# Optimization experiments

Hardware: AMD Instinct MI355X
Metric: run time of the kernel (lower is better)

The kernel has to match this reference:

```python
import jax, jax.numpy as jnp
import numpy as np

N_QUBITS = 10
N_LAYERS = 4
BATCH = 2048


def setup_inputs() -> dict:
    key = jax.random.key(0)
    k1, k2 = jax.random.split(key)
    x = jax.random.normal(k1, (BATCH, N_QUBITS), dtype=jnp.float32)
    q_params = jax.random.normal(k2, (N_LAYERS * N_QUBITS * 3,), dtype=jnp.float32) * 0.01
    return {"x": x, "q_params": q_params}


def _apply_1q(state, U, wire):
    # state: (B, 2, 2, ..., 2); U: (2, 2) complex. Applies U on `wire`.
    s = jnp.moveaxis(state, wire + 1, -1)
    s = jnp.einsum('...j,ij->...i', s, U)
    return jnp.moveaxis(s, -1, wire + 1)


def _apply_cnot(state, ctrl, tgt):
    # flip target amplitude pair where control bit == 1
    s = jnp.moveaxis(state, (ctrl + 1, tgt + 1), (-2, -1))
    s = jnp.concatenate([s[..., 0:1, :], s[..., 1:2, ::-1]], axis=-2)
    return jnp.moveaxis(s, (-2, -1), (ctrl + 1, tgt + 1))


def _forward(x, q_params):
    B = x.shape[0]
    n, L = N_QUBITS, N_LAYERS
    # --- data-encoding layer: RY(x_i)|0> = [cos(x_i/2), sin(x_i/2)] per qubit ---
    half = 0.5 * x
    amps = jnp.stack([jnp.cos(half), jnp.sin(half)], axis=-1).astype(jnp.complex64)  # (B, n, 2)
    state = amps[:, 0, :]
    for i in range(1, n):  # build product state via successive kron (loop over n_qubits only)
        state = (state[:, :, None] * amps[:, i, None, :]).reshape(B, -1)
    state = state.reshape((B,) + (2,) * n)
    # --- variational gate matrices: per (layer, qubit) fused U = RZ @ RY @ RX ---
    w = q_params.reshape(L, n, 3)
    c, s = jnp.cos(0.5 * w), jnp.sin(0.5 * w)
    cx = c[..., 0].astype(jnp.complex64); sx = s[..., 0].astype(jnp.complex64)
    cy = c[..., 1].astype(jnp.complex64); sy = s[..., 1].astype(jnp.complex64)
    ez = jnp.exp(-0.5j * w[..., 2].astype(jnp.complex64))
    zeros = jnp.zeros_like(ez)
    Urx = jnp.stack([jnp.stack([cx, -1j * sx], -1), jnp.stack([-1j * sx, cx], -1)], -2)  # (L,n,2,2)
    Ury = jnp.stack([jnp.stack([cy, -sy], -1), jnp.stack([sy, cy], -1)], -2)
    Urz = jnp.stack([jnp.stack([ez, zeros], -1), jnp.stack([zeros, jnp.conj(ez)], -1)], -2)
    U = jnp.einsum('lnab,lnbc,lncd->lnad', Urz, Ury, Urx)  # apply order: RX then RY then RZ
    # --- circuit layers ---
    for l in range(L):
        for i in range(n):
            state = _apply_1q(state, U[l, i], i)
        for i in range(n - 1):
            state = _apply_cnot(state, i, i + 1)
    # --- <Z_i> expectation values ---
    p = jnp.abs(state) ** 2  # (B, 2, ..., 2) real probabilities
    evs = []
    for i in range(n):
        axes = tuple(a for a in range(1, n + 1) if a != i + 1)
        pi = jnp.sum(p, axis=axes)  # (B, 2)
        evs.append(pi[:, 0] - pi[:, 1])
    return jnp.stack(evs, axis=-1)  # (B, n_qubits)


def reference(x, q_params):
    return _forward(x, q_params)
```

## Files before the change

### kernel.cpp

```cpp
#include <hip/hip_runtime.h>
#include <math.h>

#define NQ 10
#define NL 4
#define NGATES (NL * NQ)
#define NTHREADS 256
#define WPB 4

typedef float f32x2 __attribute__((ext_vector_type(2)));

#if __has_builtin(__builtin_amdgcn_permlane32_swap)
#define HAVE_PL32 1
#else
#define HAVE_PL32 0
#endif
#if __has_builtin(__builtin_amdgcn_permlane16_swap)
#define HAVE_PL16 1
#else
#define HAVE_PL16 0
#endif


template<int XM>
__device__ __forceinline__ float exch1(float v, bool sp32, bool sp16) {
    if constexpr (XM == 0) return v;
    int x = __float_as_int(v);
    constexpr int low = XM & 31;
    if constexpr (low == 1)       x = __builtin_amdgcn_mov_dpp(x, 0xB1, 0xF, 0xF, true);
    else if constexpr (low == 2)  x = __builtin_amdgcn_mov_dpp(x, 0x4E, 0xF, 0xF, true);
    else if constexpr (low == 3)  x = __builtin_amdgcn_mov_dpp(x, 0x1B, 0xF, 0xF, true);
    else if constexpr (low == 7)  x = __builtin_amdgcn_mov_dpp(x, 0x141, 0xF, 0xF, true);
    else if constexpr (low == 8)  x = __builtin_amdgcn_mov_dpp(x, 0x128, 0xF, 0xF, true);
    else if constexpr (low == 9)  { x = __builtin_amdgcn_mov_dpp(x, 0x128, 0xF, 0xF, true);
                                    x = __builtin_amdgcn_mov_dpp(x, 0xB1, 0xF, 0xF, true); }
    else if constexpr (low == 10) { x = __builtin_amdgcn_mov_dpp(x, 0x128, 0xF, 0xF, true);
                                    x = __builtin_amdgcn_mov_dpp(x, 0x4E, 0xF, 0xF, true); }
    else if constexpr (low == 11) { x = __builtin_amdgcn_mov_dpp(x, 0x128, 0xF, 0xF, true);
                                    x = __builtin_amdgcn_mov_dpp(x, 0x1B, 0xF, 0xF, true); }
    else if constexpr (low == 15) x = __builtin_amdgcn_mov_dpp(x, 0x140, 0xF, 0xF, true);
    else if constexpr (low == 16) {
#if HAVE_PL16
        auto r = __builtin_amdgcn_permlane16_swap((unsigned)x, (unsigned)x, false, false);
        x = sp16 ? (int)r[0] : (int)r[1];
#else
        x = __builtin_amdgcn_ds_swizzle(x, (16 << 10) | 0x1F);
#endif
    }
    else if constexpr (low != 0)  x = __builtin_amdgcn_ds_swizzle(x, (low << 10) | 0x1F);
    if constexpr ((XM & 32) != 0) {
#if HAVE_PL32
        auto r = __builtin_amdgcn_permlane32_swap((unsigned)x, (unsigned)x, false, false);
        x = sp32 ? (int)r[0] : (int)r[1];
#else
        x = __float_as_int(__shfl_xor(__int_as_float(x), 32, 64));
#endif
    }
    return __int_as_float(x);
}

template<int XM>
__device__ __forceinline__ f32x2 exch2(f32x2 v, bool sp32, bool sp16) {
    f32x2 r;
    r.x = exch1<XM>(v.x, sp32, sp16);
    r.y = exch1<XM>(v.y, sp32, sp16);
    return r;
}

__device__ __forceinline__ f32x2 cfma4(f32x2 A, f32x2 st, f32x2 B, f32x2 pst) {
    f32x2 t;
    asm("v_pk_mul_f32 %0, %1, %2 op_sel:[0,0] op_sel_hi:[0,1]\n\t"
        "v_pk_fma_f32 %0, %1, %2, %0 op_sel:[1,1,0] op_sel_hi:[1,0,1] neg_lo:[0,1,0]\n\t"
        "v_pk_fma_f32 %0, %3, %4, %0 op_sel:[0,0,0] op_sel_hi:[0,1,1]\n\t"
        "v_pk_fma_f32 %0, %3, %4, %0 op_sel:[1,1,0] op_sel_hi:[1,0,1] neg_lo:[0,1,0]"
        : "=&v"(t)
        : "v"(A), "v"(st), "v"(B), "v"(pst));
    return t;
}

template<int XM, int XR, int SL, int SR>
__device__ __forceinline__ void gate(f32x2 (&st)[16], const f32x2 (&g4)[4],
                                     int lane, bool sp32, bool sp16) {
    bool hl = (SL != 0) && ((__popc(lane & SL) & 1) != 0);
    f32x2 A0, B0, A1, B1;
    A0.x = hl ? g4[3].x : g4[0].x;  A0.y = hl ? g4[3].y : g4[0].y;
    B0.x = hl ? g4[2].x : g4[1].x;  B0.y = hl ? g4[2].y : g4[1].y;
    A1.x = hl ? g4[0].x : g4[3].x;  A1.y = hl ? g4[0].y : g4[3].y;
    B1.x = hl ? g4[1].x : g4[2].x;  B1.y = hl ? g4[1].y : g4[2].y;
    f32x2 pst[16];
    #pragma unroll
    for (int r = 0; r < 16; ++r) pst[r] = exch2<XM>(st[r ^ XR], sp32, sp16);
    #pragma unroll
    for (int r = 0; r < 16; ++r) {
        const bool p1 = (__builtin_popcount(r & SR) & 1) != 0;
        f32x2 Ar = p1 ? A1 : A0;
        f32x2 Br = p1 ? B1 : B0;
        st[r] = cfma4(Ar, st[r], Br, pst[r]);
    }
}

__device__ __forceinline__ float wht6(float v, int lane, bool sp32, bool sp16) {
    float t;
    t = exch1<1>(v, sp32, sp16);   v = (lane & 1)  ? (t - v) : (v + t);
    t = exch1<2>(v, sp32, sp16);   v = (lane & 2)  ? (t - v) : (v + t);
    t = exch1<4>(v, sp32, sp16);   v = (lane & 4)  ? (t - v) : (v + t);
    t = exch1<8>(v, sp32, sp16);   v = (lane & 8)  ? (t - v) : (v + t);
    t = exch1<16>(v, sp32, sp16);  v = (lane & 16) ? (t - v) : (v + t);
    t = exch1<32>(v, sp32, sp16);  v = (lane & 32) ? (t - v) : (v + t);
    return v;
}

__global__ __launch_bounds__(NTHREADS, 2) void qlayer_kernel(
    const float* __restrict__ x,
    const float* __restrict__ qp,
    float* __restrict__ out,
    int B)
{
    __shared__ f32x2 su[NGATES][4];

    const int t = threadIdx.x;
    if (t < NGATES) {
        float w0 = qp[t * 3 + 0], w1 = qp[t * 3 + 1], w2 = qp[t * 3 + 2];
        float cx = __cosf(0.5f * w0), sx = __sinf(0.5f * w0);
        float cy = __cosf(0.5f * w1), sy = __sinf(0.5f * w1);
        float er = __cosf(0.5f * w2), ei = -__sinf(0.5f * w2);
        float m00r =  cy * cx, m00i =  sy * sx;
        float m01r = -sy * cx, m01i = -cy * sx;
        float m10r =  sy * cx, m10i = -cy * sx;
        float m11r =  cy * cx, m11i = -sy * sx;
        f32x2 v;
        v.x = er * m00r - ei * m00i;  v.y = er * m00i + ei * m00r;  su[t][0] = v;
        v.x = er * m01r - ei * m01i;  v.y = er * m01i + ei * m01r;  su[t][1] = v;
        v.x = er * m10r + ei * m10i;  v.y = er * m10i - ei * m10r;  su[t][2] = v;
        v.x = er * m11r + ei * m11i;  v.y = er * m11i - ei * m11r;  su[t][3] = v;
    }
    __syncthreads();

    const int lane = t & 63;
    const int b = blockIdx.x * WPB + (t >> 6);
    if (b >= B) return;

    bool sp32 = false, sp16 = false;
#if HAVE_PL32
    {
        auto pr = __builtin_amdgcn_permlane32_swap((unsigned)lane, (unsigned)lane, false, false);
        sp32 = ((int)pr[0] == (lane ^ 32));
    }
#endif
#if HAVE_PL16
    {
        auto pr = __builtin_amdgcn_permlane16_swap((unsigned)lane, (unsigned)lane, false, false);
        sp16 = ((int)pr[0] == (lane ^ 16));
    }
#endif

    float c[NQ], s[NQ];
    #pragma unroll
    for (int q = 0; q < NQ; ++q) {
        float h = 0.5f * x[b * NQ + q];
        c[q] = __cosf(h);  s[q] = __sinf(h);
    }

    float lf = ((lane &  4) ? s[0] : c[0]) * ((lane & 32) ? s[1] : c[1]) *
               ((lane & 16) ? s[2] : c[2]) * ((lane &  8) ? s[7] : c[7]) *
               ((lane &  2) ? s[8] : c[8]) * ((lane &  1) ? s[9] : c[9]);
    f32x2 st[16];
    #pragma unroll
    for (int r = 0; r < 16; ++r) {
        st[r].x = lf * ((r & 8) ? s[3] : c[3]) * ((r & 4) ? s[4] : c[4]) *
                       ((r & 2) ? s[5] : c[5]) * ((r & 1) ? s[6] : c[6]);
        st[r].y = 0.0f;
    }

#define PREFETCH(L)                                                   \
    f32x2 cf[NQ][4];                                                  \
    _Pragma("unroll")                                                 \
    for (int q = 0; q < NQ; ++q) {                                    \
        cf[q][0] = su[(L)*NQ + q][0];  cf[q][1] = su[(L)*NQ + q][1];  \
        cf[q][2] = su[(L)*NQ + q][2];  cf[q][3] = su[(L)*NQ + q][3];  \
    }
#define GATE(Q, XM, XR, SLm, SRm) \
    gate<XM, XR, SLm, SRm>(st, cf[Q], lane, sp32, sp16);

    {
        PREFETCH(0)
        GATE(0, 4,0, 4,0)     GATE(1, 32,0, 32,0)  GATE(2, 16,0, 16,0)
        GATE(3, 0,8, 0,8)     GATE(4, 0,4, 0,4)    GATE(5, 0,2, 0,2)
        GATE(6, 0,1, 0,1)     GATE(7, 8,0, 8,0)    GATE(8, 2,0, 2,0)
        GATE(9, 1,0, 1,0)
    }
    {
        PREFETCH(1)
        GATE(0, 36,0, 4,0)    GATE(1, 48,0, 36,0)  GATE(2, 16,8, 52,0)
        GATE(3, 0,12, 52,8)   GATE(4, 0,6, 52,12)  GATE(5, 0,3, 52,14)
        GATE(6, 8,1, 52,15)   GATE(7, 10,0, 60,15) GATE(8, 3,0, 62,15)
        GATE(9, 1,0, 63,15)
    }
    {
        PREFETCH(2)
        GATE(0, 20,0, 4,0)    GATE(1, 32,8, 32,0)  GATE(2, 16,4, 20,0)
        GATE(3, 0,10, 32,8)   GATE(4, 0,5, 20,4)   GATE(5, 8,2, 32,10)
        GATE(6, 2,1, 20,5)    GATE(7, 9,0, 40,10)  GATE(8, 2,0, 22,5)
        GATE(9, 1,0, 41,10)
    }
    {
        PREFETCH(3)
        GATE(0, 52,8, 4,0)    GATE(1, 48,12, 36,0) GATE(2, 16,14, 48,0)
        GATE(3, 0,15, 16,8)   GATE(4, 8,7, 4,12)   GATE(5, 10,3, 36,6)
        GATE(6, 11,1, 48,3)   GATE(7, 11,0, 24,9)  GATE(8, 3,0, 14,12)
        GATE(9, 1,0, 39,6)
    }
#undef GATE
#undef PREFETCH

    float p[16];
    #pragma unroll
    for (int r = 0; r < 16; ++r) p[r] = st[r].x * st[r].x + st[r].y * st[r].y;
    float a[8], f8 = 0.0f;
    #pragma unroll
    for (int r = 0; r < 8; ++r) { a[r] = p[r] + p[r + 8]; f8 += p[r] - p[r + 8]; }
    float c4[4], f4 = 0.0f;
    #pragma unroll
    for (int r = 0; r < 4; ++r) { c4[r] = a[r] + a[r + 4]; f4 += a[r] - a[r + 4]; }
    float e2[2], f2 = 0.0f;
    #pragma unroll
    for (int r = 0; r < 2; ++r) { e2[r] = c4[r] + c4[r + 2]; f2 += c4[r] - c4[r + 2]; }
    float P  = e2[0] + e2[1];
    float f1 = e2[0] - e2[1];

    float wP = wht6(P,  lane, sp32, sp16);
    float w8 = wht6(f8, lane, sp32, sp16);
    float w4 = wht6(f4, lane, sp32, sp16);
    float w2 = wht6(f2, lane, sp32, sp16);
    float w1 = wht6(f1, lane, sp32, sp16);

    float* o = out + b * NQ;
    if (lane ==  4) { o[0] = wP; o[4] = w4; }
    if (lane == 32) { o[1] = wP; o[5] = w2; }
    if (lane == 16) { o[2] = wP; o[6] = w1; }
    if (lane ==  0) { o[3] = w8; }
    if (lane ==  8) { o[7] = w8; }
    if (lane ==  6) { o[8] = w4; }
    if (lane == 33) { o[9] = w2; }
}

extern "C" void kernel_launch(void* const* d_in, const int* in_sizes, int n_in,
                              void* d_out, int out_size, void* d_ws, size_t ws_size,
                              hipStream_t stream) {
    const float* x  = (const float*)d_in[0];
    const float* qp = (const float*)d_in[1];
    float* out = (float*)d_out;
    const int B = in_sizes[0] / NQ;
    const int blocks = (B + WPB - 1) / WPB;
    qlayer_kernel<<<blocks, NTHREADS, 0, stream>>>(x, qp, out, B);
}
```

Measured before the change: 77.23 us.

## Split each batch state across two wavefronts with LDS exchange for qubit 3

Each 1024-amplitude state vector is now held by two wavefronts (8 complex amplitudes per lane instead of 16). Qubit 3 is mapped to the wave index, and gates touching it exchange halves through shared memory with block barriers. Final expectation values are combined across the pair through LDS. The goal is to cut register pressure (launch bounds raised to 4 blocks) and double parallelism. The cost is many __syncthreads and extra LDS traffic per cross-wave gate.

Result: slower. 80.23 us (+3.9%).

```diff
diff --git a/kernel.cpp b/kernel.cpp
--- a/kernel.cpp
+++ b/kernel.cpp
@@ -5,7 +5,6 @@
 #define NL 4
 #define NGATES (NL * NQ)
 #define NTHREADS 256
-#define WPB 4
 
 typedef float f32x2 __attribute__((ext_vector_type(2)));
 
@@ -77,24 +76,50 @@
     return t;
 }
 
-template<int XM, int XR, int SL, int SR>
-__device__ __forceinline__ void gate(f32x2 (&st)[16], const f32x2 (&g4)[4],
-                                     int lane, bool sp32, bool sp16) {
-    bool hl = (SL != 0) && ((__popc(lane & SL) & 1) != 0);
-    f32x2 A0, B0, A1, B1;
+__device__ __forceinline__ void mkSel(const f32x2 (&g4)[4], bool hl,
+                                      f32x2& A0, f32x2& B0, f32x2& A1, f32x2& B1) {
     A0.x = hl ? g4[3].x : g4[0].x;  A0.y = hl ? g4[3].y : g4[0].y;
     B0.x = hl ? g4[2].x : g4[1].x;  B0.y = hl ? g4[2].y : g4[1].y;
     A1.x = hl ? g4[0].x : g4[3].x;  A1.y = hl ? g4[0].y : g4[3].y;
     B1.x = hl ? g4[1].x : g4[2].x;  B1.y = hl ? g4[1].y : g4[2].y;
-    f32x2 pst[16];
-    #pragma unroll
-    for (int r = 0; r < 16; ++r) pst[r] = exch2<XM>(st[r ^ XR], sp32, sp16);
-    #pragma unroll
-    for (int r = 0; r < 16; ++r) {
+}
+
+template<int XM, int XR, int SL, int SR, int SW>
+__device__ __forceinline__ void gate(f32x2 (&st)[8], const f32x2 (&g4)[4],
+                                     int lane, int W, bool sp32, bool sp16) {
+    int hli = (__popc(lane & SL) & 1) ^ (SW ? W : 0);
+    bool hl = hli != 0;
+    f32x2 A0, B0, A1, B1;
+    mkSel(g4, hl, A0, B0, A1, B1);
+    f32x2 pst[8];
+    #pragma unroll
+    for (int r = 0; r < 8; ++r) pst[r] = exch2<XM>(st[r ^ XR], sp32, sp16);
+    #pragma unroll
+    for (int r = 0; r < 8; ++r) {
         const bool p1 = (__builtin_popcount(r & SR) & 1) != 0;
-        f32x2 Ar = p1 ? A1 : A0;
-        f32x2 Br = p1 ? B1 : B0;
-        st[r] = cfma4(Ar, st[r], Br, pst[r]);
+        st[r] = cfma4(p1 ? A1 : A0, st[r], p1 ? B1 : B0, pst[r]);
+    }
+}
+
+template<int XL, int XR, int SL, int SR, int SW, int BUF>
+__device__ __forceinline__ void xgate(f32x2 (&st)[8], const f32x2 (&g4)[4],
+                                      int lane, int wv, int W, f32x2* sb) {
+    f32x2* mb = sb + (((BUF * 4 + wv) * 64 + lane) * 8);
+    #pragma unroll
+    for (int r = 0; r < 8; ++r) mb[r] = st[r];
+    __syncthreads();
+    int hli = (__popc(lane & SL) & 1) ^ (SW ? W : 0);
+    bool hl = hli != 0;
+    f32x2 A0, B0, A1, B1;
+    mkSel(g4, hl, A0, B0, A1, B1);
+    const f32x2* pb = sb + (((BUF * 4 + (wv ^ 1)) * 64 + (lane ^ XL)) * 8);
+    f32x2 pst[8];
+    #pragma unroll
+    for (int r = 0; r < 8; ++r) pst[r] = pb[r ^ XR];
+    #pragma unroll
+    for (int r = 0; r < 8; ++r) {
+        const bool p1 = (__builtin_popcount(r & SR) & 1) != 0;
+        st[r] = cfma4(p1 ? A1 : A0, st[r], p1 ? B1 : B0, pst[r]);
     }
 }
 
@@ -109,13 +134,15 @@
     return v;
 }
 
-__global__ __launch_bounds__(NTHREADS, 2) void qlayer_kernel(
+__global__ __launch_bounds__(NTHREADS, 4) void qlayer_kernel(
     const float* __restrict__ x,
     const float* __restrict__ qp,
     float* __restrict__ out,
     int B)
 {
     __shared__ f32x2 su[NGATES][4];
+    __shared__ f32x2 sbuf[2][4][64][8];
+    __shared__ float evb[4][10];
 
     const int t = threadIdx.x;
     if (t < NGATES) {
@@ -136,8 +163,11 @@
     __syncthreads();
 
     const int lane = t & 63;
-    const int b = blockIdx.x * WPB + (t >> 6);
-    if (b >= B) return;
+    const int wv = t >> 6;
+    const int W = wv & 1;
+    const int b0 = blockIdx.x * 2 + (wv >> 1);
+    const bool bok = (b0 < B);
+    const int bx = bok ? b0 : 0;
 
     bool sp32 = false, sp16 = false;
 #if HAVE_PL32
@@ -156,91 +186,82 @@
     float c[NQ], s[NQ];
     #pragma unroll
     for (int q = 0; q < NQ; ++q) {
-        float h = 0.5f * x[b * NQ + q];
+        float h = 0.5f * x[bx * NQ + q];
         c[q] = __cosf(h);  s[q] = __sinf(h);
     }
 
     float lf = ((lane &  4) ? s[0] : c[0]) * ((lane & 32) ? s[1] : c[1]) *
-               ((lane & 16) ? s[2] : c[2]) * ((lane &  8) ? s[7] : c[7]) *
-               ((lane &  2) ? s[8] : c[8]) * ((lane &  1) ? s[9] : c[9]);
-    f32x2 st[16];
-    #pragma unroll
-    for (int r = 0; r < 16; ++r) {
-        st[r].x = lf * ((r & 8) ? s[3] : c[3]) * ((r & 4) ? s[4] : c[4]) *
-                       ((r & 2) ? s[5] : c[5]) * ((r & 1) ? s[6] : c[6]);
+               ((lane & 16) ? s[2] : c[2]) * (W ? s[3] : c[3]) *
+               ((lane &  8) ? s[7] : c[7]) * ((lane &  2) ? s[8] : c[8]) *
+               ((lane &  1) ? s[9] : c[9]);
+    f32x2 st[8];
+    #pragma unroll
+    for (int r = 0; r < 8; ++r) {
+        st[r].x = lf * ((r & 4) ? s[4] : c[4]) * ((r & 2) ? s[5] : c[5]) *
+                       ((r & 1) ? s[6] : c[6]);
         st[r].y = 0.0f;
     }
 
-#define PREFETCH(L)                                                   \
-    f32x2 cf[NQ][4];                                                  \
-    _Pragma("unroll")                                                 \
-    for (int q = 0; q < NQ; ++q) {                                    \
-        cf[q][0] = su[(L)*NQ + q][0];  cf[q][1] = su[(L)*NQ + q][1];  \
-        cf[q][2] = su[(L)*NQ + q][2];  cf[q][3] = su[(L)*NQ + q][3];  \
-    }
-#define GATE(Q, XM, XR, SLm, SRm) \
-    gate<XM, XR, SLm, SRm>(st, cf[Q], lane, sp32, sp16);
-
-    {
-        PREFETCH(0)
-        GATE(0, 4,0, 4,0)     GATE(1, 32,0, 32,0)  GATE(2, 16,0, 16,0)
-        GATE(3, 0,8, 0,8)     GATE(4, 0,4, 0,4)    GATE(5, 0,2, 0,2)
-        GATE(6, 0,1, 0,1)     GATE(7, 8,0, 8,0)    GATE(8, 2,0, 2,0)
-        GATE(9, 1,0, 1,0)
-    }
-    {
-        PREFETCH(1)
-        GATE(0, 36,0, 4,0)    GATE(1, 48,0, 36,0)  GATE(2, 16,8, 52,0)
-        GATE(3, 0,12, 52,8)   GATE(4, 0,6, 52,12)  GATE(5, 0,3, 52,14)
-        GATE(6, 8,1, 52,15)   GATE(7, 10,0, 60,15) GATE(8, 3,0, 62,15)
-        GATE(9, 1,0, 63,15)
-    }
-    {
-        PREFETCH(2)
-        GATE(0, 20,0, 4,0)    GATE(1, 32,8, 32,0)  GATE(2, 16,4, 20,0)
-        GATE(3, 0,10, 32,8)   GATE(4, 0,5, 20,4)   GATE(5, 8,2, 32,10)
-        GATE(6, 2,1, 20,5)    GATE(7, 9,0, 40,10)  GATE(8, 2,0, 22,5)
-        GATE(9, 1,0, 41,10)
-    }
-    {
-        PREFETCH(3)
-        GATE(0, 52,8, 4,0)    GATE(1, 48,12, 36,0) GATE(2, 16,14, 48,0)
-        GATE(3, 0,15, 16,8)   GATE(4, 8,7, 4,12)   GATE(5, 10,3, 36,6)
-        GATE(6, 11,1, 48,3)   GATE(7, 11,0, 24,9)  GATE(8, 3,0, 14,12)
-        GATE(9, 1,0, 39,6)
-    }
-#undef GATE
-#undef PREFETCH
-
-    float p[16];
-    #pragma unroll
-    for (int r = 0; r < 16; ++r) p[r] = st[r].x * st[r].x + st[r].y * st[r].y;
-    float a[8], f8 = 0.0f;
-    #pragma unroll
-    for (int r = 0; r < 8; ++r) { a[r] = p[r] + p[r + 8]; f8 += p[r] - p[r + 8]; }
-    float c4[4], f4 = 0.0f;
-    #pragma unroll
-    for (int r = 0; r < 4; ++r) { c4[r] = a[r] + a[r + 4]; f4 += a[r] - a[r + 4]; }
-    float e2[2], f2 = 0.0f;
-    #pragma unroll
-    for (int r = 0; r < 2; ++r) { e2[r] = c4[r] + c4[r + 2]; f2 += c4[r] - c4[r + 2]; }
-    float P  = e2[0] + e2[1];
-    float f1 = e2[0] - e2[1];
+    f32x2* sb = &sbuf[0][0][0][0];
+#define G(L, Q, XM, XR, SLm, SRm, SWm) \
+    gate<XM, XR, SLm, SRm, SWm>(st, su[(L)*NQ+(Q)], lane, W, sp32, sp16);
+#define XG(L, Q, XL, XR, SLm, SRm, SWm, BUF) \
+    xgate<XL, XR, SLm, SRm, SWm, BUF>(st, su[(L)*NQ+(Q)], lane, wv, W, sb);
+
+    G (0,0, 4,0, 4,0,0)    G (0,1, 32,0, 32,0,0)  G (0,2, 16,0, 16,0,0)
+    XG(0,3, 0,0, 0,0,1, 0)
+    G (0,4, 0,4, 0,4,0)    G (0,5, 0,2, 0,2,0)    G (0,6, 0,1, 0,1,0)
+    G (0,7, 8,0, 8,0,0)    G (0,8, 2,0, 2,0,0)    G (0,9, 1,0, 1,0,0)
+    G (1,0, 36,0, 4,0,0)   G (1,1, 48,0, 36,0,0)
+    XG(1,2, 16,0, 52,0,0, 1)
+    XG(1,3, 0,4, 52,0,1, 0)
+    G (1,4, 0,6, 52,4,1)   G (1,5, 0,3, 52,6,1)   G (1,6, 8,1, 52,7,1)
+    G (1,7, 10,0, 60,7,1)  G (1,8, 3,0, 62,7,1)   G (1,9, 1,0, 63,7,1)
+    G (2,0, 20,0, 4,0,0)
+    XG(2,1, 32,0, 32,0,0, 1)
+    G (2,2, 16,4, 20,0,0)
+    XG(2,3, 0,2, 32,0,1, 0)
+    G (2,4, 0,5, 20,4,0)   G (2,5, 8,2, 32,2,1)   G (2,6, 2,1, 20,5,0)
+    G (2,7, 9,0, 40,2,1)   G (2,8, 2,0, 22,5,0)   G (2,9, 1,0, 41,2,1)
+    XG(3,0, 52,0, 4,0,0, 1)
+    XG(3,1, 48,4, 36,0,0, 0)
+    XG(3,2, 16,6, 48,0,0, 1)
+    XG(3,3, 0,7, 16,0,1, 0)
+    G (3,4, 8,7, 4,4,1)    G (3,5, 10,3, 36,6,0)  G (3,6, 2,1, 48,3,0)
+    G (3,7, 11,0, 24,1,1)  G (3,8, 3,0, 14,4,1)   G (3,9, 1,0, 39,6,0)
+#undef G
+#undef XG
+
+    float p[8];
+    #pragma unroll
+    for (int r = 0; r < 8; ++r) p[r] = st[r].x * st[r].x + st[r].y * st[r].y;
+    float a4[4], f4 = 0.0f;
+    #pragma unroll
+    for (int r = 0; r < 4; ++r) { a4[r] = p[r] + p[r + 4]; f4 += p[r] - p[r + 4]; }
+    float a2[2], f2 = 0.0f;
+    #pragma unroll
+    for (int r = 0; r < 2; ++r) { a2[r] = a4[r] + a4[r + 2]; f2 += a4[r] - a4[r + 2]; }
+    float P  = a2[0] + a2[1];
+    float f1 = a2[0] - a2[1];
 
     float wP = wht6(P,  lane, sp32, sp16);
-    float w8 = wht6(f8, lane, sp32, sp16);
     float w4 = wht6(f4, lane, sp32, sp16);
     float w2 = wht6(f2, lane, sp32, sp16);
     float w1 = wht6(f1, lane, sp32, sp16);
 
-    float* o = out + b * NQ;
-    if (lane ==  4) { o[0] = wP; o[4] = w4; }
-    if (lane == 32) { o[1] = wP; o[5] = w2; }
-    if (lane == 16) { o[2] = wP; o[6] = w1; }
-    if (lane ==  0) { o[3] = w8; }
-    if (lane ==  8) { o[7] = w8; }
-    if (lane ==  6) { o[8] = w4; }
-    if (lane == 33) { o[9] = w2; }
+    if (lane ==  4) { evb[wv][0] = wP; evb[wv][4] = w4; }
+    if (lane == 32) { evb[wv][1] = wP; evb[wv][5] = w2; }
+    if (lane == 16) { evb[wv][2] = wP; evb[wv][6] = w1; }
+    if (lane ==  0) { evb[wv][3] = wP; }
+    if (lane ==  8) { evb[wv][7] = wP; }
+    if (lane ==  6) { evb[wv][8] = w4; }
+    if (lane == 33) { evb[wv][9] = w2; }
+    __syncthreads();
+
+    if (bok && (wv & 1) == 0 && lane < NQ) {
+        float sgn = (lane == 3 || lane == 7) ? -1.0f : 1.0f;
+        out[b0 * NQ + lane] = evb[wv][lane] + sgn * evb[wv + 1][lane];
+    }
 }
 
 extern "C" void kernel_launch(void* const* d_in, const int* in_sizes, int n_in,
@@ -250,6 +271,6 @@
     const float* qp = (const float*)d_in[1];
     float* out = (float*)d_out;
     const int B = in_sizes[0] / NQ;
-    const int blocks = (B + WPB - 1) / WPB;
+    const int blocks = (B + 1) / 2;
     qlayer_kernel<<<blocks, NTHREADS, 0, stream>>>(x, qp, out, B);
 }
```
